# Performance work log

Hardware: AMD Instinct MI355X
Metric: run time of the kernel (lower is better)

## Reference

```python
import jax, jax.numpy as jnp
import numpy as np

B, T, C, D, P = 8, 512, 32, 128, 1024
EPS = 1e-5

def setup_inputs() -> dict:
    key = jax.random.key(0)
    ks = jax.random.split(key, 11)
    s = 1.0 / np.sqrt(D)
    inp = {
        'x': jax.random.normal(ks[0], (B, T, C, D), jnp.float32),
        'x_mask': jax.random.randint(ks[1], (B, T, C), 0, 2) == 1,
        'p_mask': jax.random.randint(ks[2], (B, T, C), 0, 2) == 1,
        'pos': jax.random.randint(ks[3], (B, T, C), 0, P),
        'pe': jax.random.normal(ks[4], (P, D // 2, 2), jnp.float32),  # complex rpe as [re, im]
        'imp': jax.random.randint(ks[5], (B, T), 0, C),
        'idx_c': jax.random.randint(ks[6], (B, T, C), 0, C),
        'wq_w': jax.random.normal(ks[7], (D, D), jnp.float32) * s,
        'wq_b': jnp.zeros((D,), jnp.float32),
        'wk_w': jax.random.normal(ks[8], (D, D), jnp.float32) * s,
        'wk_b': jnp.zeros((D,), jnp.float32),
        'wv_w': jax.random.normal(ks[9], (D, D), jnp.float32) * s,
        'wv_b': jnp.zeros((D,), jnp.float32),
        'ls_gamma': 1e-5 * jnp.ones((D,), jnp.float32),
        'ln_gamma': jnp.ones((D,), jnp.float32),
        'ln_beta': jnp.zeros((D,), jnp.float32),
    }
    return inp


def _rotate(z, r):
    # z: (b,t,c,d) real; r: (b,t,c,d/2,2) complex multiplier [re,im]
    b, t, c, d = z.shape
    zr = z.reshape(b, t, c, d // 2, 2)
    re = zr[..., 0] * r[..., 0] - zr[..., 1] * r[..., 1]
    im = zr[..., 0] * r[..., 1] + zr[..., 1] * r[..., 0]
    return jnp.stack([re, im], axis=-1).reshape(b, t, c, d)


def reference(x, x_mask, p_mask, pos, pe, imp, idx_c,
              wq_w, wq_b, wk_w, wk_b, wv_w, wv_b,
              ls_gamma, ln_gamma, ln_beta):
    b, t, c, d = x.shape
    # channel selection gather: where x_mask, use per-token important channel
    imp_rep = jnp.broadcast_to(imp[:, :, None], (b, t, c))
    idx = jnp.where(x_mask, imp_rep, idx_c)            # (b,t,c)
    xg = jnp.take_along_axis(x, idx[..., None], axis=2)  # (b,t,c,d)
    # QKV projections (torch Linear: x @ W.T + b)
    q = xg @ wq_w.T + wq_b
    k = xg @ wk_w.T + wk_b
    v = xg @ wv_w.T + wv_b
    # relative PE complex rotation on q,k
    r = pe[pos]                                        # (b,t,c,d/2,2)
    q = _rotate(q, r)
    k = _rotate(k, r)
    # (b,c,t,d) layout; channel acts as head
    qt = q.transpose(0, 2, 1, 3)
    kt = k.transpose(0, 2, 1, 3)
    vt = v.transpose(0, 2, 1, 3)
    scores = jnp.einsum('bcqd,bckd->bcqk', qt, kt) / jnp.sqrt(jnp.float32(d))
    pm = p_mask.transpose(0, 2, 1)                     # (b,c,t)
    mask = pm[:, :, :, None] | pm[:, :, None, :]       # (b,c,t,t)
    attn = jax.nn.softmax(jnp.where(mask, -jnp.inf, scores), axis=-1)
    attn = jnp.nan_to_num(attn)
    xm = x_mask.transpose(0, 2, 1)                     # (b,c,t)
    weight = jnp.where(xm, 1.0 / t, 1.0)
    out = jnp.einsum('bcmn,bcnd->bmcd', attn * weight[:, :, None, :], vt)  # (b,t,c,d)
    # norm_first=False: LN(x + layer_scale(out))
    y = x + ls_gamma * out
    mu = jnp.mean(y, axis=-1, keepdims=True)
    var = jnp.mean(jnp.square(y - mu), axis=-1, keepdims=True)
    return (y - mu) / jnp.sqrt(var + EPS) * ln_gamma + ln_beta
```

## Files before the change

### kernel.cpp

```cpp
#include <hip/hip_runtime.h>
#include <hip/hip_bf16.h>

#define Bb 8
#define Tt 512
#define Cc 32
#define Dd 128
#define SCALE 0.08838834764831845f
#define SROW 520

typedef unsigned int u32;
typedef __hip_bfloat16 bf16;
typedef __attribute__((ext_vector_type(8))) short short8;
typedef __attribute__((ext_vector_type(4))) short short4v;
typedef __attribute__((ext_vector_type(4))) float floatx4;

__device__ __forceinline__ short f2bf(float f) {
    __hip_bfloat16 h = __float2bfloat16(f);
    return *(short*)&h;
}
__device__ __forceinline__ float bf2f(short s) {
    return __uint_as_float(((u32)(unsigned short)s) << 16);
}

__global__ __launch_bounds__(256)
void k_wconv(const float* __restrict__ wq, const float* __restrict__ wk,
             const float* __restrict__ wv, short* __restrict__ Wb)
{
    int g = blockIdx.x * 256 + threadIdx.x;
    int mat = g >> 14, rem = g & 16383;
    const float* src = (mat == 0) ? wq : (mat == 1) ? wk : wv;
    Wb[g] = f2bf(src[rem]);
}

__global__ __launch_bounds__(256)
void k_qkvm(const float* __restrict__ x, const int* __restrict__ xm,
            const int* __restrict__ pos, const float* __restrict__ pe,
            const int* __restrict__ imp, const int* __restrict__ idxc,
            const short* __restrict__ Wb,
            const float* __restrict__ bq, const float* __restrict__ bk,
            const float* __restrict__ bv,
            short* __restrict__ qb, short* __restrict__ kb, short* __restrict__ vb)
{
    const int R0  = blockIdx.x * 64;
    const int b   = R0 >> 14;
    const int t0  = (R0 >> 5) & 511;
    const int tid = threadIdx.x;
    const int w    = tid >> 6;
    const int lane = tid & 63;
    const int quad = lane >> 4;
    const int m    = lane & 15;

    __shared__ short xg[64 * 136];
    __shared__ short ot[64 * 392];

#pragma unroll
    for (int i = 0; i < 8; ++i) {
        int u   = tid + i * 256;
        int row = u >> 5, seg = u & 31;
        int R   = R0 + row;
        int idx = xm[R] ? imp[R >> 5] : idxc[R];
        float4 v = *(const float4*)(x + ((long)(R >> 5) * Cc + idx) * Dd + seg * 4);
        short4v s = {f2bf(v.x), f2bf(v.y), f2bf(v.z), f2bf(v.w)};
        *(short4v*)&xg[row * 136 + seg * 4] = s;
    }

    short8 wf[6][4];
    float  bias_v[6];
#pragma unroll
    for (int mat = 0; mat < 3; ++mat) {
        const float* bp = (mat == 0) ? bq : (mat == 1) ? bk : bv;
#pragma unroll
        for (int h = 0; h < 2; ++h) {
            int sl = mat * 2 + h;
            int ct = h * 4 + w;
            bias_v[sl] = bp[ct * 16 + m];
#pragma unroll
            for (int kb = 0; kb < 4; ++kb)
                wf[sl][kb] = *(const short8*)(Wb + ((long)mat * 128 + ct * 16 + m) * 128
                                              + kb * 32 + quad * 8);
        }
    }
    __syncthreads();

    for (int rt = 0; rt < 4; ++rt) {
        short8 af[4];
#pragma unroll
        for (int kb = 0; kb < 4; ++kb)
            af[kb] = *(const short8*)&xg[(rt * 16 + m) * 136 + kb * 32 + quad * 8];

        floatx4 acc[6];
#pragma unroll
        for (int sl = 0; sl < 6; ++sl) acc[sl] = (floatx4){0.f, 0.f, 0.f, 0.f};
#pragma unroll
        for (int kb = 0; kb < 4; ++kb)
#pragma unroll
            for (int sl = 0; sl < 6; ++sl)
                acc[sl] = __builtin_amdgcn_mfma_f32_16x16x32_bf16(af[kb], wf[sl][kb], acc[sl], 0, 0, 0);

        int po[4];
#pragma unroll
        for (int r = 0; r < 4; ++r) po[r] = pos[R0 + rt * 16 + quad * 4 + r];

#pragma unroll
        for (int sl = 0; sl < 6; ++sl) {
            int mat = sl >> 1;
            int ct  = (sl & 1) * 4 + w;
            int d   = ct * 16 + m;
#pragma unroll
            for (int r = 0; r < 4; ++r) {
                float v = acc[sl][r] + bias_v[sl];
                float p = __shfl_xor(v, 1, 64);
                if (mat < 2) {
                    const float* rp = pe + ((long)po[r] * (Dd / 2) + (d >> 1)) * 2;
                    float r0 = rp[0], r1 = rp[1];
                    v = (d & 1) ? fmaf(p, r1, v * r0) : fmaf(v, r0, -(p * r1));
                }
                ot[(rt * 16 + quad * 4 + r) * 392 + mat * 128 + d] = f2bf(v);
            }
        }
    }
    __syncthreads();

    short* const mats[3] = {qb, kb, vb};
#pragma unroll
    for (int mat = 0; mat < 3; ++mat) {
        short* dst = mats[mat];
#pragma unroll
        for (int i = 0; i < 4; ++i) {
            int g = tid + i * 256;
            int n = g >> 4, off = (g & 15) * 8;
            int c = n & 31, tl = n >> 5;
            *(short8*)(dst + (((long)(b * Cc + c) * Tt) + t0 + tl) * Dd + off) =
                *(const short8*)&ot[n * 392 + mat * 128 + off];
        }
    }
}

__global__ __launch_bounds__(256)
void k_vt(const short* __restrict__ vb, short* __restrict__ vt)
{
    const int head = blockIdx.y;
    const int t0   = blockIdx.x * 64;
    const int tid  = threadIdx.x;

    __shared__ short tile[64 * 136];

    const short* src = vb + ((long)head * Tt + t0) * Dd;
#pragma unroll
    for (int i = 0; i < 4; ++i) {
        int u = tid + i * 256;
        int row = u >> 4, col = (u & 15) * 8;
        *(short8*)&tile[row * 136 + col] = *(const short8*)(src + row * Dd + col);
    }
    __syncthreads();

    short* dst = vt + (long)head * Dd * Tt + t0;
#pragma unroll
    for (int i = 0; i < 4; ++i) {
        int u = tid + i * 256;
        int d = u >> 3, t8 = (u & 7) * 8;
        short8 v;
#pragma unroll
        for (int j = 0; j < 8; ++j) v[j] = tile[(t8 + j) * 136 + d];
        *(short8*)(dst + (long)d * Tt + t8) = v;
    }
}

__global__ __launch_bounds__(256)
void k_attn(const short* __restrict__ qb, const short* __restrict__ kbp,
            const short* __restrict__ vtp, const float* __restrict__ x,
            const int* __restrict__ xm, const int* __restrict__ pm,
            const float* __restrict__ lsg, const float* __restrict__ lng,
            const float* __restrict__ lnb, float* __restrict__ out)
{
    const int head = blockIdx.y;
    const int b    = head >> 5;
    const int c    = head & 31;
    const int qt0  = blockIdx.x * 32;
    const int tid  = threadIdx.x;
    const int w    = tid >> 6;
    const int lane = tid & 63;
    const int quad = lane >> 4;
    const int m    = lane & 15;

    __shared__ short S[32 * SROW];
    __shared__ short KV[128 * 72];
    __shared__ float wk_[Tt];
    __shared__ float pk_[Tt];
    __shared__ float rlS[32];
    __shared__ float ps1[4][32];
    __shared__ float ps2[4][32];
    __shared__ float mrs[32][2];

    for (int i = tid; i < Tt; i += 256) {
        int base = (b * Tt + i) * Cc + c;
        wk_[i] = xm[base] ? (1.0f / Tt) : 1.0f;
        pk_[i] = pm[base] ? 1.0f : 0.0f;
    }

    short8 qf[2][4];
#pragma unroll
    for (int qt = 0; qt < 2; ++qt)
#pragma unroll
        for (int kb = 0; kb < 4; ++kb)
            qf[qt][kb] = *(const short8*)(qb + ((long)head * Tt + qt0 + qt * 16 + m) * Dd
                                          + kb * 32 + quad * 8);

    for (int ch = 0; ch < 8; ++ch) {
        __syncthreads();
        const short* src = kbp + ((long)head * Tt + ch * 64) * Dd;
#pragma unroll
        for (int i = 0; i < 4; ++i) {
            int u = tid + i * 256;
            int row = u >> 4, col = (u & 15) * 8;
            *(short8*)&KV[row * 136 + col] = *(const short8*)(src + row * Dd + col);
        }
        __syncthreads();

        floatx4 sc0 = {0.f, 0.f, 0.f, 0.f}, sc1 = {0.f, 0.f, 0.f, 0.f};
#pragma unroll
        for (int kb = 0; kb < 4; ++kb) {
            short8 bk = *(const short8*)&KV[(w * 16 + m) * 136 + kb * 32 + quad * 8];
            sc0 = __builtin_amdgcn_mfma_f32_16x16x32_bf16(qf[0][kb], bk, sc0, 0, 0, 0);
            sc1 = __builtin_amdgcn_mfma_f32_16x16x32_bf16(qf[1][kb], bk, sc1, 0, 0, 0);
        }
        int kt = ch * 64 + w * 16 + m;
        bool masked = pk_[kt] > 0.5f;
#pragma unroll
        for (int r = 0; r < 4; ++r) {
            float v0 = masked ? -1e30f : sc0[r] * SCALE;
            float v1 = masked ? -1e30f : sc1[r] * SCALE;
            S[(quad * 4 + r) * SROW + kt]      = f2bf(v0);
            S[(16 + quad * 4 + r) * SROW + kt] = f2bf(v1);
        }
    }
    __syncthreads();

    {
        int qi = tid >> 3, part = tid & 7;
        float mx = -1e30f;
        for (int j = 0; j < 64; ++j) mx = fmaxf(mx, bf2f(S[qi * SROW + j * 8 + part]));
        mx = fmaxf(mx, __shfl_xor(mx, 1, 64));
        mx = fmaxf(mx, __shfl_xor(mx, 2, 64));
        mx = fmaxf(mx, __shfl_xor(mx, 4, 64));
        float l = 0.f;
        for (int j = 0; j < 64; ++j) {
            int kt = j * 8 + part;
            float s = bf2f(S[qi * SROW + kt]);
            float e = (s <= -1e29f) ? 0.f : __expf(s - mx);
            S[qi * SROW + kt] = f2bf(e * wk_[kt]);
            l += e;
        }
        l += __shfl_xor(l, 1, 64);
        l += __shfl_xor(l, 2, 64);
        l += __shfl_xor(l, 4, 64);
        if (part == 0)
            rlS[qi] = (l > 0.f && pk_[qt0 + qi] < 0.5f) ? 1.0f / l : 0.f;
    }
    __syncthreads();

    floatx4 oa[2][2];
#pragma unroll
    for (int qt = 0; qt < 2; ++qt)
#pragma unroll
        for (int dt = 0; dt < 2; ++dt) oa[qt][dt] = (floatx4){0.f, 0.f, 0.f, 0.f};

    for (int ch = 0; ch < 8; ++ch) {
        __syncthreads();
        const short* vsrc = vtp + (long)head * Dd * Tt + ch * 64;
#pragma unroll
        for (int i = 0; i < 4; ++i) {
            int u = tid + i * 256;
            int d = u >> 3, t8 = (u & 7) * 8;
            *(short8*)&KV[d * 72 + t8] = *(const short8*)(vsrc + (long)d * Tt + t8);
        }
        __syncthreads();

#pragma unroll
        for (int kb = 0; kb < 2; ++kb) {
            short8 bv0 = *(const short8*)&KV[((w * 2 + 0) * 16 + m) * 72 + kb * 32 + quad * 8];
            short8 bv1 = *(const short8*)&KV[((w * 2 + 1) * 16 + m) * 72 + kb * 32 + quad * 8];
#pragma unroll
            for (int qt = 0; qt < 2; ++qt) {
                short8 ap = *(const short8*)&S[(qt * 16 + m) * SROW + ch * 64 + kb * 32 + quad * 8];
                oa[qt][0] = __builtin_amdgcn_mfma_f32_16x16x32_bf16(ap, bv0, oa[qt][0], 0, 0, 0);
                oa[qt][1] = __builtin_amdgcn_mfma_f32_16x16x32_bf16(ap, bv1, oa[qt][1], 0, 0, 0);
            }
        }
    }

    float yv[2][2][4];
    float s1[2][4], s2[2][4];
#pragma unroll
    for (int qt = 0; qt < 2; ++qt)
#pragma unroll
        for (int r = 0; r < 4; ++r) { s1[qt][r] = 0.f; s2[qt][r] = 0.f; }

#pragma unroll
    for (int qt = 0; qt < 2; ++qt)
#pragma unroll
        for (int dt = 0; dt < 2; ++dt) {
            int d = (w * 2 + dt) * 16 + m;
            float lg = lsg[d];
#pragma unroll
            for (int r = 0; r < 4; ++r) {
                int row = qt * 16 + quad * 4 + r;
                int t = qt0 + row;
                float val = oa[qt][dt][r] * rlS[row];
                float y = x[(((long)b * Tt + t) * Cc + c) * Dd + d] + lg * val;
                yv[qt][dt][r] = y;
                s1[qt][r] += y;
                s2[qt][r] += y * y;
            }
        }
#pragma unroll
    for (int qt = 0; qt < 2; ++qt)
#pragma unroll
        for (int r = 0; r < 4; ++r) {
            float a = s1[qt][r], bb = s2[qt][r];
            a += __shfl_xor(a, 1, 64); bb += __shfl_xor(bb, 1, 64);
            a += __shfl_xor(a, 2, 64); bb += __shfl_xor(bb, 2, 64);
            a += __shfl_xor(a, 4, 64); bb += __shfl_xor(bb, 4, 64);
            a += __shfl_xor(a, 8, 64); bb += __shfl_xor(bb, 8, 64);
            if (m == 0) {
                ps1[w][qt * 16 + quad * 4 + r] = a;
                ps2[w][qt * 16 + quad * 4 + r] = bb;
            }
        }
    __syncthreads();
    if (tid < 32) {
        float a = 0.f, bb = 0.f;
#pragma unroll
        for (int wv = 0; wv < 4; ++wv) { a += ps1[wv][tid]; bb += ps2[wv][tid]; }
        float mean = a * (1.0f / Dd);
        float var  = bb * (1.0f / Dd) - mean * mean;
        mrs[tid][0] = mean;
        mrs[tid][1] = rsqrtf(var + 1e-5f);
    }
    __syncthreads();

#pragma unroll
    for (int qt = 0; qt < 2; ++qt)
#pragma unroll
        for (int dt = 0; dt < 2; ++dt) {
            int d = (w * 2 + dt) * 16 + m;
            float g = lng[d], be = lnb[d];
#pragma unroll
            for (int r = 0; r < 4; ++r) {
                int row = qt * 16 + quad * 4 + r;
                int t = qt0 + row;
                out[(((long)b * Tt + t) * Cc + c) * Dd + d] =
                    (yv[qt][dt][r] - mrs[row][0]) * mrs[row][1] * g + be;
            }
        }
}

extern "C" void kernel_launch(void* const* d_in, const int* in_sizes, int n_in,
                              void* d_out, int out_size, void* d_ws, size_t ws_size,
                              hipStream_t stream) {
    const float* x    = (const float*)d_in[0];
    const int* xmask  = (const int*)d_in[1];
    const int* pmask  = (const int*)d_in[2];
    const int* pos    = (const int*)d_in[3];
    const float* pe   = (const float*)d_in[4];
    const int* imp    = (const int*)d_in[5];
    const int* idxc   = (const int*)d_in[6];
    const float* wq_w = (const float*)d_in[7];
    const float* wq_b = (const float*)d_in[8];
    const float* wk_w = (const float*)d_in[9];
    const float* wk_b = (const float*)d_in[10];
    const float* wv_w = (const float*)d_in[11];
    const float* wv_b = (const float*)d_in[12];
    const float* lsg  = (const float*)d_in[13];
    const float* lng  = (const float*)d_in[14];
    const float* lnb  = (const float*)d_in[15];
    float* out = (float*)d_out;

    size_t n = (size_t)Bb * Cc * Tt * Dd;
    short* qb = (short*)d_ws;
    short* kb = qb + n;
    short* vb = kb + n;
    short* vt = vb + n;
    short* Wb = vt + n;

    k_wconv<<<dim3(3 * Dd * Dd / 256), dim3(256), 0, stream>>>(wq_w, wk_w, wv_w, Wb);
    k_qkvm<<<dim3(Bb * Tt * Cc / 64), dim3(256), 0, stream>>>(
        x, xmask, pos, pe, imp, idxc, Wb, wq_b, wk_b, wv_b, qb, kb, vb);
    k_vt<<<dim3(Tt / 64, Bb * Cc), dim3(256), 0, stream>>>(vb, vt);
    k_attn<<<dim3(Tt / 32, Bb * Cc), dim3(256), 0, stream>>>(
        qb, kb, vt, x, xmask, pmask, lsg, lng, lnb, out);
}
```

Baseline: 369.6 us.

## Fold scale into Q, key weights into V transpose, read K/V directly from global

Pre-multiplies Q by the softmax scale in the projection kernel and applies the per-key x_mask weight to V during the transpose, so the attention kernel no longer scales scores or weights probabilities. The attention kernel drops its LDS staging of K and V tiles and the barriers around it, loading MFMA operands straight from global memory. The padding mask is packed into ballot bitmasks in shared memory, and launch bounds request more occupancy. Direct global loads depend on cache reuse across waves, and rounding V after weighting adds a little bf16 error.

```diff
diff --git a/kernel.cpp b/kernel.cpp
--- a/kernel.cpp
+++ b/kernel.cpp
@@ -114,6 +114,7 @@
                     const float* rp = pe + ((long)po[r] * (Dd / 2) + (d >> 1)) * 2;
                     float r0 = rp[0], r1 = rp[1];
                     v = (d & 1) ? fmaf(p, r1, v * r0) : fmaf(v, r0, -(p * r1));
+                    if (mat == 0) v *= SCALE;
                 }
                 ot[(rt * 16 + quad * 4 + r) * 392 + mat * 128 + d] = f2bf(v);
             }
@@ -137,13 +138,20 @@
 }
 
 __global__ __launch_bounds__(256)
-void k_vt(const short* __restrict__ vb, short* __restrict__ vt)
+void k_vt(const short* __restrict__ vb, const int* __restrict__ xm,
+          short* __restrict__ vt)
 {
     const int head = blockIdx.y;
+    const int b    = head >> 5;
+    const int c    = head & 31;
     const int t0   = blockIdx.x * 64;
     const int tid  = threadIdx.x;
 
     __shared__ short tile[64 * 136];
+    __shared__ float wks[64];
+
+    if (tid < 64)
+        wks[tid] = xm[((long)b * Tt + t0 + tid) * Cc + c] ? (1.0f / Tt) : 1.0f;
 
     const short* src = vb + ((long)head * Tt + t0) * Dd;
 #pragma unroll
@@ -161,15 +169,16 @@
         int d = u >> 3, t8 = (u & 7) * 8;
         short8 v;
 #pragma unroll
-        for (int j = 0; j < 8; ++j) v[j] = tile[(t8 + j) * 136 + d];
+        for (int j = 0; j < 8; ++j)
+            v[j] = f2bf(bf2f(tile[(t8 + j) * 136 + d]) * wks[t8 + j]);
         *(short8*)(dst + (long)d * Tt + t8) = v;
     }
 }
 
-__global__ __launch_bounds__(256)
+__global__ __launch_bounds__(256, 4)
 void k_attn(const short* __restrict__ qb, const short* __restrict__ kbp,
             const short* __restrict__ vtp, const float* __restrict__ x,
-            const int* __restrict__ xm, const int* __restrict__ pm,
+            const int* __restrict__ pm,
             const float* __restrict__ lsg, const float* __restrict__ lng,
             const float* __restrict__ lnb, float* __restrict__ out)
 {
@@ -184,18 +193,21 @@
     const int m    = lane & 15;
 
     __shared__ short S[32 * SROW];
-    __shared__ short KV[128 * 72];
-    __shared__ float wk_[Tt];
-    __shared__ float pk_[Tt];
+    __shared__ u32   pkbits[16];
     __shared__ float rlS[32];
     __shared__ float ps1[4][32];
     __shared__ float ps2[4][32];
     __shared__ float mrs[32][2];
 
-    for (int i = tid; i < Tt; i += 256) {
-        int base = (b * Tt + i) * Cc + c;
-        wk_[i] = xm[base] ? (1.0f / Tt) : 1.0f;
-        pk_[i] = pm[base] ? 1.0f : 0.0f;
+#pragma unroll
+    for (int p = 0; p < 2; ++p) {
+        int i = p * 256 + tid;
+        bool v = pm[((long)b * Tt + i) * Cc + c] != 0;
+        unsigned long long bal = __ballot(v);
+        if (lane == 0) {
+            pkbits[p * 8 + w * 2]     = (u32)bal;
+            pkbits[p * 8 + w * 2 + 1] = (u32)(bal >> 32);
+        }
     }
 
     short8 qf[2][4];
@@ -205,33 +217,25 @@
         for (int kb = 0; kb < 4; ++kb)
             qf[qt][kb] = *(const short8*)(qb + ((long)head * Tt + qt0 + qt * 16 + m) * Dd
                                           + kb * 32 + quad * 8);
-
+    __syncthreads();
+
+#pragma unroll 2
     for (int ch = 0; ch < 8; ++ch) {
-        __syncthreads();
-        const short* src = kbp + ((long)head * Tt + ch * 64) * Dd;
-#pragma unroll
-        for (int i = 0; i < 4; ++i) {
-            int u = tid + i * 256;
-            int row = u >> 4, col = (u & 15) * 8;
-            *(short8*)&KV[row * 136 + col] = *(const short8*)(src + row * Dd + col);
-        }
-        __syncthreads();
-
+        const short* kp = kbp + ((long)head * Tt + ch * 64 + w * 16 + m) * Dd + quad * 8;
         floatx4 sc0 = {0.f, 0.f, 0.f, 0.f}, sc1 = {0.f, 0.f, 0.f, 0.f};
 #pragma unroll
         for (int kb = 0; kb < 4; ++kb) {
-            short8 bk = *(const short8*)&KV[(w * 16 + m) * 136 + kb * 32 + quad * 8];
+            short8 bk = *(const short8*)(kp + kb * 32);
             sc0 = __builtin_amdgcn_mfma_f32_16x16x32_bf16(qf[0][kb], bk, sc0, 0, 0, 0);
             sc1 = __builtin_amdgcn_mfma_f32_16x16x32_bf16(qf[1][kb], bk, sc1, 0, 0, 0);
         }
         int kt = ch * 64 + w * 16 + m;
-        bool masked = pk_[kt] > 0.5f;
+        u32 wbits = pkbits[ch * 2 + ((w * 16 + m) >> 5)];
+        bool masked = (wbits >> ((w * 16 + m) & 31)) & 1;
 #pragma unroll
         for (int r = 0; r < 4; ++r) {
-            float v0 = masked ? -1e30f : sc0[r] * SCALE;
-            float v1 = masked ? -1e30f : sc1[r] * SCALE;
-            S[(quad * 4 + r) * SROW + kt]      = f2bf(v0);
-            S[(16 + quad * 4 + r) * SROW + kt] = f2bf(v1);
+            S[(quad * 4 + r) * SROW + kt]      = f2bf(masked ? -1e30f : sc0[r]);
+            S[(16 + quad * 4 + r) * SROW + kt] = f2bf(masked ? -1e30f : sc1[r]);
         }
     }
     __syncthreads();
@@ -248,14 +252,16 @@
             int kt = j * 8 + part;
             float s = bf2f(S[qi * SROW + kt]);
             float e = (s <= -1e29f) ? 0.f : __expf(s - mx);
-            S[qi * SROW + kt] = f2bf(e * wk_[kt]);
+            S[qi * SROW + kt] = f2bf(e);
             l += e;
         }
         l += __shfl_xor(l, 1, 64);
         l += __shfl_xor(l, 2, 64);
         l += __shfl_xor(l, 4, 64);
-        if (part == 0)
-            rlS[qi] = (l > 0.f && pk_[qt0 + qi] < 0.5f) ? 1.0f / l : 0.f;
+        if (part == 0) {
+            bool qmask = (pkbits[blockIdx.x] >> qi) & 1;
+            rlS[qi] = (l > 0.f && !qmask) ? 1.0f / l : 0.f;
+        }
     }
     __syncthreads();
 
@@ -265,24 +271,17 @@
 #pragma unroll
         for (int dt = 0; dt < 2; ++dt) oa[qt][dt] = (floatx4){0.f, 0.f, 0.f, 0.f};
 
+    const short* vbase = vtp + (long)head * Dd * Tt;
+#pragma unroll 2
     for (int ch = 0; ch < 8; ++ch) {
-        __syncthreads();
-        const short* vsrc = vtp + (long)head * Dd * Tt + ch * 64;
-#pragma unroll
-        for (int i = 0; i < 4; ++i) {
-            int u = tid + i * 256;
-            int d = u >> 3, t8 = (u & 7) * 8;
-            *(short8*)&KV[d * 72 + t8] = *(const short8*)(vsrc + (long)d * Tt + t8);
-        }
-        __syncthreads();
-
 #pragma unroll
         for (int kb = 0; kb < 2; ++kb) {
-            short8 bv0 = *(const short8*)&KV[((w * 2 + 0) * 16 + m) * 72 + kb * 32 + quad * 8];
-            short8 bv1 = *(const short8*)&KV[((w * 2 + 1) * 16 + m) * 72 + kb * 32 + quad * 8];
+            int tcol = ch * 64 + kb * 32 + quad * 8;
+            short8 bv0 = *(const short8*)(vbase + ((long)((w * 2 + 0) * 16 + m)) * Tt + tcol);
+            short8 bv1 = *(const short8*)(vbase + ((long)((w * 2 + 1) * 16 + m)) * Tt + tcol);
 #pragma unroll
             for (int qt = 0; qt < 2; ++qt) {
-                short8 ap = *(const short8*)&S[(qt * 16 + m) * SROW + ch * 64 + kb * 32 + quad * 8];
+                short8 ap = *(const short8*)&S[(qt * 16 + m) * SROW + tcol];
                 oa[qt][0] = __builtin_amdgcn_mfma_f32_16x16x32_bf16(ap, bv0, oa[qt][0], 0, 0, 0);
                 oa[qt][1] = __builtin_amdgcn_mfma_f32_16x16x32_bf16(ap, bv1, oa[qt][1], 0, 0, 0);
             }
@@ -386,7 +385,7 @@
     k_wconv<<<dim3(3 * Dd * Dd / 256), dim3(256), 0, stream>>>(wq_w, wk_w, wv_w, Wb);
     k_qkvm<<<dim3(Bb * Tt * Cc / 64), dim3(256), 0, stream>>>(
         x, xmask, pos, pe, imp, idxc, Wb, wq_b, wk_b, wv_b, qb, kb, vb);
-    k_vt<<<dim3(Tt / 64, Bb * Cc), dim3(256), 0, stream>>>(vb, vt);
+    k_vt<<<dim3(Tt / 64, Bb * Cc), dim3(256), 0, stream>>>(vb, xmask, vt);
     k_attn<<<dim3(Tt / 32, Bb * Cc), dim3(256), 0, stream>>>(
-        qb, kb, vt, x, xmask, pmask, lsg, lng, lnb, out);
-}
+        qb, kb, vt, x, pmask, lsg, lng, lnb, out);
+}
```

After: 351.8 us. 1.05x faster.
